# Kernel optimization log

Measured on AMD Instinct MI355X. Metric: run time of the kernel, lower is better.

Reference implementation:

```python
import jax, jax.numpy as jnp
import numpy as np

B, N, TF, DM = 16, 4096, 512, 1024

def next_fast_len(n):
    # smallest 5-smooth number >= n (matches scipy.fftpack.next_fast_len)
    while True:
        m = n
        for p in (2, 3, 5):
            while m % p == 0:
                m //= p
        if m == 1:
            return n
        n += 1

def conv1d_fft(x, weights):
    # x: (..., N, F), weights: (M,); causal exponentially-weighted correlation
    n = x.shape[-2]
    m = weights.shape[-1]
    L = next_fast_len(n + m - 1)
    f_x = jnp.fft.rfft(x, n=L, axis=-2)                 # (..., Lr, F) complex
    f_w = jnp.fft.rfft(weights, n=L, axis=-1)           # (Lr,)
    out = jnp.fft.irfft(f_x * jnp.conj(f_w)[..., None], L, axis=-2)
    out = jnp.roll(out, -1, axis=-2)
    return out[..., L - n:, :]                           # last N along seq axis

def setup_inputs() -> dict:
    key = jax.random.key(0)
    ks = jax.random.split(key, 8)
    inp = {
        "x": jax.random.normal(ks[0], (B, N, TF), dtype=jnp.float32),
        "latent_growth": jax.random.normal(ks[1], (B, N, DM), dtype=jnp.float32),
        "latent_seasonal": jax.random.normal(ks[2], (B, N, DM), dtype=jnp.float32),
        "alpha": jnp.zeros((1,), dtype=jnp.float32),  # nn.Parameter(torch.Tensor([0.0]))
        "w_growth": jax.random.normal(ks[3], (TF, DM), dtype=jnp.float32) / np.sqrt(DM),
        "b_growth": jnp.zeros((TF,), dtype=jnp.float32),
        "w_seasonal": jax.random.normal(ks[4], (TF, DM), dtype=jnp.float32) / np.sqrt(DM),
        "b_seasonal": jnp.zeros((TF,), dtype=jnp.float32),
    }
    return inp

def reference(x, latent_growth, latent_seasonal, alpha, w_growth, b_growth, w_seasonal, b_seasonal):
    n = x.shape[1]
    a = jax.nn.sigmoid(alpha)[0]
    powers = jnp.arange(n, dtype=x.dtype)[::-1]          # flipped arange
    seasonal = jnp.einsum('bnd,fd->bnf', latent_seasonal, w_seasonal) + b_seasonal
    aes_weights = a * (1.0 - a) ** powers                # alpha*(1-alpha)^k EMA kernel
    seasonal_normalized_term = conv1d_fft(x - seasonal, aes_weights)
    # NOTE: the original module computes `growth` but does not use it in the output
    growth = jnp.einsum('bnd,fd->bnf', latent_growth, w_growth) + b_growth
    growth_term = conv1d_fft(x, aes_weights)
    return seasonal_normalized_term + growth_term
```

## Files before the change

### kernel.cpp

```cpp
#include <hip/hip_runtime.h>
#include <math.h>

#define B_DIM 16
#define N_SEQ 4096
#define TF_DIM 512
#define DM_DIM 1024
#define CHUNK 128
#define NCHUNK (N_SEQ / CHUNK)
#define NKT (DM_DIM / 32)

typedef __attribute__((ext_vector_type(4))) float f32x4;
typedef __attribute__((ext_vector_type(8))) short bf16x8;
typedef unsigned short u16;
typedef unsigned int u32;

__device__ __forceinline__ u16 f2bf(float f) {
    u32 u = __builtin_bit_cast(u32, f);
    u += 0x7fffu + ((u >> 16) & 1u);
    return (u16)(u >> 16);
}

__device__ __forceinline__ void gload16(const float* g, float* l) {
    __builtin_amdgcn_global_load_lds(
        (const __attribute__((address_space(1))) void*)g,
        (__attribute__((address_space(3))) void*)l,
        16, 0, 0);
}

__device__ __forceinline__ u32 cvtpk(float lo, float hi) {
    u32 r;
    asm("v_cvt_pk_bf16_f32 %0, %1, %2" : "=v"(r) : "v"(lo), "v"(hi));
    return r;
}

__device__ __forceinline__ bf16x8 pack8(f32x4 v0, f32x4 v1) {
    union { u32 u[4]; bf16x8 v; } p;
    p.u[0] = cvtpk(v0[0], v0[1]);
    p.u[1] = cvtpk(v0[2], v0[3]);
    p.u[2] = cvtpk(v1[0], v1[1]);
    p.u[3] = cvtpk(v1[2], v1[3]);
    return p.v;
}

__global__ __launch_bounds__(256, 2)
void gemm_u_kernel(const float* __restrict__ x,
                   const float* __restrict__ ls,
                   const float* __restrict__ wmat,
                   const float* __restrict__ bias,
                   const float* __restrict__ alpha,
                   u16* __restrict__ u,
                   float* __restrict__ e)
{
    __shared__ float As[2][4096];
    __shared__ float Ws[2][4096];
    __shared__ float red[2][4][16];

    const int tid  = threadIdx.x;
    const int f0   = blockIdx.x * 128;
    const int row0 = blockIdx.y * 128;

    const int lane = tid & 63;
    const int wid  = tid >> 6;
    const int wm = wid >> 1, wn = wid & 1;
    const int l15 = lane & 15, l4 = lane >> 4;

    const int sr = wid * 32 + (lane >> 3);
    const int sc = ((lane & 7) ^ ((lane >> 3) & 7)) * 4;
    const float* aSrc = ls   + (size_t)(row0 + sr) * DM_DIM + sc;
    const float* wSrc = wmat + (size_t)(f0   + sr) * DM_DIM + sc;
    const int ldsb = wid * 1024;

#define STAGE(BUF, KT) do {                                              \
        const int _ko = (KT) * 32;                                       \
        gload16(aSrc + _ko,         &As[BUF][ldsb]);                     \
        gload16(aSrc + _ko +  8192, &As[BUF][ldsb + 256]);               \
        gload16(aSrc + _ko + 16384, &As[BUF][ldsb + 512]);               \
        gload16(aSrc + _ko + 24576, &As[BUF][ldsb + 768]);               \
        gload16(wSrc + _ko,         &Ws[BUF][ldsb]);                     \
        gload16(wSrc + _ko +  8192, &Ws[BUF][ldsb + 256]);               \
        gload16(wSrc + _ko + 16384, &Ws[BUF][ldsb + 512]);               \
        gload16(wSrc + _ko + 24576, &Ws[BUF][ldsb + 768]);               \
    } while (0)

    const int xr   = (l15 & 7) << 2;
    const int aoff = (wm * 64 + l15) * 32 + ((l4 * 8) ^ xr);
    const int woff = (wn * 64 + l15) * 32 + ((l4 * 8) ^ xr);

    f32x4 acc[4][4];
#pragma unroll
    for (int i = 0; i < 4; ++i)
#pragma unroll
        for (int j = 0; j < 4; ++j) acc[i][j] = (f32x4){0.f, 0.f, 0.f, 0.f};

#define COMPUTE(BUF) do {                                                \
        const float* _Ab = &As[BUF][0];                                  \
        const float* _Wb = &Ws[BUF][0];                                  \
        bf16x8 _af[4], _wf[4];                                           \
        _Pragma("unroll")                                                \
        for (int i = 0; i < 4; ++i) {                                    \
            f32x4 _v0 = *(const f32x4*)(_Ab + (aoff + i * 512));         \
            f32x4 _v1 = *(const f32x4*)(_Ab + ((aoff ^ 4) + i * 512));   \
            _af[i] = pack8(_v0, _v1);                                    \
        }                                                                \
        _Pragma("unroll")                                                \
        for (int i = 0; i < 4; ++i) {                                    \
            f32x4 _v0 = *(const f32x4*)(_Wb + (woff + i * 512));         \
            f32x4 _v1 = *(const f32x4*)(_Wb + ((woff ^ 4) + i * 512));   \
            _wf[i] = pack8(_v0, _v1);                                    \
        }                                                                \
        _Pragma("unroll")                                                \
        for (int mi = 0; mi < 4; ++mi)                                   \
        _Pragma("unroll")                                                \
        for (int ni = 0; ni < 4; ++ni)                                   \
            acc[mi][ni] = __builtin_amdgcn_mfma_f32_16x16x32_bf16(       \
                _af[mi], _wf[ni], acc[mi][ni], 0, 0, 0);                 \
    } while (0)

    STAGE(0, 0);
    __syncthreads();

#pragma unroll 1
    for (int kt = 0; kt < NKT; kt += 2) {
        if (kt + 1 < NKT) STAGE(1, kt + 1);
        COMPUTE(0);
        __syncthreads();
        if (kt + 2 < NKT) STAGE(0, kt + 2);
        COMPUTE(1);
        __syncthreads();
    }

    const float a = 1.0f / (1.0f + expf(-alpha[0]));
    const float c = 1.0f - a;
    const float l2c = log2f(c);

    float bia[4];
#pragma unroll
    for (int ni = 0; ni < 4; ++ni) bia[ni] = bias[f0 + wn * 64 + ni * 16 + l15];

    float epart[4] = {0.f, 0.f, 0.f, 0.f};

#pragma unroll
    for (int mi = 0; mi < 4; ++mi) {
#pragma unroll
        for (int j = 0; j < 4; ++j) {
            const int r = wm * 64 + mi * 16 + l4 * 4 + j;
            const size_t rb = (size_t)(row0 + r) * TF_DIM;
            const float wgt = (r == CHUNK - 1)
                                  ? a
                                  : a * exp2f((float)(CHUNK - 1 - r) * l2c);
#pragma unroll
            for (int ni = 0; ni < 4; ++ni) {
                const int f = f0 + wn * 64 + ni * 16 + l15;
                const float uval = 2.0f * x[rb + f] - (acc[mi][ni][j] + bia[ni]);
                u[rb + f] = f2bf(uval);
                epart[ni] = fmaf(wgt, uval, epart[ni]);
            }
        }
    }

#pragma unroll
    for (int ni = 0; ni < 4; ++ni) {
        epart[ni] += __shfl_xor(epart[ni], 16, 64);
        epart[ni] += __shfl_xor(epart[ni], 32, 64);
    }
    if (wm == 1 && l4 == 0) {
#pragma unroll
        for (int ni = 0; ni < 4; ++ni) red[wn][ni][l15] = epart[ni];
    }
    __syncthreads();
    if (wm == 0 && l4 == 0) {
#pragma unroll
        for (int ni = 0; ni < 4; ++ni) {
            const int f = f0 + wn * 64 + ni * 16 + l15;
            e[(size_t)blockIdx.y * TF_DIM + f] = epart[ni] + red[wn][ni][l15];
        }
    }
}

__global__ __launch_bounds__(256)
void ema_carry(const float* __restrict__ e, const float* __restrict__ alpha,
               float* __restrict__ carry)
{
    const int idx = blockIdx.x * 256 + threadIdx.x;
    const int f = idx & (TF_DIM - 1);
    const int b = idx >> 9;
    const float a = 1.0f / (1.0f + expf(-alpha[0]));
    const float c = 1.0f - a;
    const float cC = exp2f((float)CHUNK * log2f(c));
    const size_t base = (size_t)b * NCHUNK * TF_DIM + f;
    float Y = 0.0f;
    carry[base] = 0.0f;
    for (int ch = 1; ch < NCHUNK; ++ch) {
        Y = fmaf(cC, Y, e[base + (size_t)(ch - 1) * TF_DIM]);
        carry[base + (size_t)ch * TF_DIM] = Y;
    }
}

__global__ __launch_bounds__(256)
void ema_apply(const u16* __restrict__ u, const float* __restrict__ carry,
               const float* __restrict__ alpha, float* __restrict__ out)
{
    const int bc = blockIdx.x;
    const int tid = threadIdx.x;
    const float a = 1.0f / (1.0f + expf(-alpha[0]));
    const float c = 1.0f - a;
    float y0 = carry[(size_t)bc * TF_DIM + 2 * tid];
    float y1 = carry[(size_t)bc * TF_DIM + 2 * tid + 1];
    const u32* up = (const u32*)(u + (size_t)bc * CHUNK * TF_DIM) + tid;
    float2*    op = (float2*)(out + (size_t)bc * CHUNK * TF_DIM) + tid;
#pragma unroll 4
    for (int j = 0; j < CHUNK; ++j) {
        const u32 w = up[(size_t)j * (TF_DIM / 2)];
        const float u0 = __builtin_bit_cast(float, (w & 0xffffu) << 16);
        const float u1 = __builtin_bit_cast(float, (w >> 16) << 16);
        y0 = fmaf(c, y0, a * u0);
        y1 = fmaf(c, y1, a * u1);
        op[(size_t)j * (TF_DIM / 2)] = make_float2(y0, y1);
    }
}

extern "C" void kernel_launch(void* const* d_in, const int* in_sizes, int n_in,
                              void* d_out, int out_size, void* d_ws, size_t ws_size,
                              hipStream_t stream) {
    const float* x     = (const float*)d_in[0];
    const float* ls    = (const float*)d_in[2];
    const float* alpha = (const float*)d_in[3];
    const float* wmat  = (const float*)d_in[6];
    const float* bias  = (const float*)d_in[7];
    float* out = (float*)d_out;

    u16*   u     = (u16*)d_ws;
    float* e     = (float*)(u + (size_t)B_DIM * N_SEQ * TF_DIM);
    float* carry = e + (size_t)B_DIM * NCHUNK * TF_DIM;

    dim3 g1(TF_DIM / 128, B_DIM * N_SEQ / 128);
    gemm_u_kernel<<<g1, 256, 0, stream>>>(x, ls, wmat, bias, alpha, u, e);

    ema_carry<<<(B_DIM * TF_DIM) / 256, 256, 0, stream>>>(e, alpha, carry);
    ema_apply<<<B_DIM * NCHUNK, 256, 0, stream>>>(u, carry, alpha, out);
}
```

Baseline: 279.0 us.

## Pre-convert GEMM operands to bf16 in a separate pass and remap block order

Adds a conversion kernel that writes latent_seasonal and the seasonal weight matrix as bf16 into workspace. The GEMM then streams bf16 tiles directly into LDS with a new swizzle, dropping the per-iteration fp32-to-bf16 packing and halving LDS and global traffic inside the main loop. Blocks are linearised and remapped so groups of eight row tiles share the four feature tiles, for better L2 reuse of activation rows. Barriers become explicit vmcnt drains. The cost is an extra full pass that reads 256MB of fp32 activations and writes 128MB of bf16, which may outweigh the savings in a GEMM that is bandwidth-bound on reading those activations.

```diff
diff --git a/kernel.cpp b/kernel.cpp
--- a/kernel.cpp
+++ b/kernel.cpp
@@ -20,71 +20,93 @@
     return (u16)(u >> 16);
 }
 
-__device__ __forceinline__ void gload16(const float* g, float* l) {
-    __builtin_amdgcn_global_load_lds(
-        (const __attribute__((address_space(1))) void*)g,
-        (__attribute__((address_space(3))) void*)l,
-        16, 0, 0);
-}
-
 __device__ __forceinline__ u32 cvtpk(float lo, float hi) {
     u32 r;
     asm("v_cvt_pk_bf16_f32 %0, %1, %2" : "=v"(r) : "v"(lo), "v"(hi));
     return r;
 }
 
-__device__ __forceinline__ bf16x8 pack8(f32x4 v0, f32x4 v1) {
-    union { u32 u[4]; bf16x8 v; } p;
-    p.u[0] = cvtpk(v0[0], v0[1]);
-    p.u[1] = cvtpk(v0[2], v0[3]);
-    p.u[2] = cvtpk(v1[0], v1[1]);
-    p.u[3] = cvtpk(v1[2], v1[3]);
-    return p.v;
+__device__ __forceinline__ void gload16(const u16* g, u16* l) {
+    __builtin_amdgcn_global_load_lds(
+        (const __attribute__((address_space(1))) void*)g,
+        (__attribute__((address_space(3))) void*)l, 16, 0, 0);
+}
+
+#define SYNC_DRAIN() asm volatile("s_waitcnt vmcnt(0)\n\ts_barrier" ::: "memory")
+
+__global__ __launch_bounds__(256)
+void cvt_bf16(const float* __restrict__ ls, const float* __restrict__ wm,
+              u16* __restrict__ lsb, u16* __restrict__ wmb)
+{
+    const size_t LSG = (size_t)B_DIM * N_SEQ * DM_DIM / 4;
+    const size_t i = (size_t)blockIdx.x * 256 + threadIdx.x;
+    const float* src;
+    u16* dst;
+    if (i < LSG) { src = ls + i * 4; dst = lsb + i * 4; }
+    else         { const size_t j = i - LSG; src = wm + j * 4; dst = wmb + j * 4; }
+    const f32x4 v = *(const f32x4*)src;
+    u32* d = (u32*)dst;
+    d[0] = cvtpk(v[0], v[1]);
+    d[1] = cvtpk(v[2], v[3]);
 }
 
 __global__ __launch_bounds__(256, 2)
 void gemm_u_kernel(const float* __restrict__ x,
-                   const float* __restrict__ ls,
-                   const float* __restrict__ wmat,
+                   const u16* __restrict__ lsb,
+                   const u16* __restrict__ wmb,
                    const float* __restrict__ bias,
                    const float* __restrict__ alpha,
                    u16* __restrict__ u,
                    float* __restrict__ e)
 {
-    __shared__ float As[2][4096];
-    __shared__ float Ws[2][4096];
+    __shared__ u16 As[2][4096];
+    __shared__ u16 Ws[2][4096];
     __shared__ float red[2][4][16];
 
-    const int tid  = threadIdx.x;
-    const int f0   = blockIdx.x * 128;
-    const int row0 = blockIdx.y * 128;
+    const int tid = threadIdx.x;
+
+    const int s  = blockIdx.x;
+    const int kk = s >> 3;
+    const int fb = kk & 3;
+    const int rp = (s & 7) + ((kk >> 2) << 3);
+    const int f0   = fb * 128;
+    const int row0 = rp * 128;
 
     const int lane = tid & 63;
     const int wid  = tid >> 6;
     const int wm = wid >> 1, wn = wid & 1;
     const int l15 = lane & 15, l4 = lane >> 4;
 
-    const int sr = wid * 32 + (lane >> 3);
-    const int sc = ((lane & 7) ^ ((lane >> 3) & 7)) * 4;
-    const float* aSrc = ls   + (size_t)(row0 + sr) * DM_DIM + sc;
-    const float* wSrc = wmat + (size_t)(f0   + sr) * DM_DIM + sc;
-    const int ldsb = wid * 1024;
+    const int G0 = wid * 128 + lane;
+    const int G1 = G0 + 64;
+    int row_a, slot_a, row_b, slot_b;
+    { const int r = G0 >> 2;
+      row_a  = (r & ~1) | ((r ^ (G0 >> 4)) & 1);
+      slot_a = (G0 & 3) ^ (row_a & 3); }
+    { const int r = G1 >> 2;
+      row_b  = (r & ~1) | ((r ^ (G1 >> 4)) & 1);
+      slot_b = (G1 & 3) ^ (row_b & 3); }
+
+    const u16* aSrc0 = lsb + (size_t)(row0 + row_a) * DM_DIM + slot_a * 8;
+    const u16* aSrc1 = lsb + (size_t)(row0 + row_b) * DM_DIM + slot_b * 8;
+    const u16* wSrc0 = wmb + (size_t)(f0 + row_a) * DM_DIM + slot_a * 8;
+    const u16* wSrc1 = wmb + (size_t)(f0 + row_b) * DM_DIM + slot_b * 8;
 
 #define STAGE(BUF, KT) do {                                              \
-        const int _ko = (KT) * 32;                                       \
-        gload16(aSrc + _ko,         &As[BUF][ldsb]);                     \
-        gload16(aSrc + _ko +  8192, &As[BUF][ldsb + 256]);               \
-        gload16(aSrc + _ko + 16384, &As[BUF][ldsb + 512]);               \
-        gload16(aSrc + _ko + 24576, &As[BUF][ldsb + 768]);               \
-        gload16(wSrc + _ko,         &Ws[BUF][ldsb]);                     \
-        gload16(wSrc + _ko +  8192, &Ws[BUF][ldsb + 256]);               \
-        gload16(wSrc + _ko + 16384, &Ws[BUF][ldsb + 512]);               \
-        gload16(wSrc + _ko + 24576, &Ws[BUF][ldsb + 768]);               \
+        const int _o = (KT) * 32;                                        \
+        gload16(aSrc0 + _o, &As[BUF][wid * 1024]);                       \
+        gload16(aSrc1 + _o, &As[BUF][wid * 1024 + 512]);                 \
+        gload16(wSrc0 + _o, &Ws[BUF][wid * 1024]);                       \
+        gload16(wSrc1 + _o, &Ws[BUF][wid * 1024 + 512]);                 \
     } while (0)
 
-    const int xr   = (l15 & 7) << 2;
-    const int aoff = (wm * 64 + l15) * 32 + ((l4 * 8) ^ xr);
-    const int woff = (wn * 64 + l15) * 32 + ((l4 * 8) ^ xr);
+    int rofa[4], rofw[4];
+    const int rxor = (l15 & 7) << 3;
+#pragma unroll
+    for (int i = 0; i < 4; ++i) {
+        rofa[i] = ((wm * 64 + i * 16 + l15) * 32 + l4 * 8) ^ rxor;
+        rofw[i] = ((wn * 64 + i * 16 + l15) * 32 + l4 * 8) ^ rxor;
+    }
 
     f32x4 acc[4][4];
 #pragma unroll
@@ -93,20 +115,13 @@
         for (int j = 0; j < 4; ++j) acc[i][j] = (f32x4){0.f, 0.f, 0.f, 0.f};
 
 #define COMPUTE(BUF) do {                                                \
-        const float* _Ab = &As[BUF][0];                                  \
-        const float* _Wb = &Ws[BUF][0];                                  \
+        const u16* _Ab = As[BUF];                                        \
+        const u16* _Wb = Ws[BUF];                                        \
         bf16x8 _af[4], _wf[4];                                           \
         _Pragma("unroll")                                                \
         for (int i = 0; i < 4; ++i) {                                    \
-            f32x4 _v0 = *(const f32x4*)(_Ab + (aoff + i * 512));         \
-            f32x4 _v1 = *(const f32x4*)(_Ab + ((aoff ^ 4) + i * 512));   \
-            _af[i] = pack8(_v0, _v1);                                    \
-        }                                                                \
-        _Pragma("unroll")                                                \
-        for (int i = 0; i < 4; ++i) {                                    \
-            f32x4 _v0 = *(const f32x4*)(_Wb + (woff + i * 512));         \
-            f32x4 _v1 = *(const f32x4*)(_Wb + ((woff ^ 4) + i * 512));   \
-            _wf[i] = pack8(_v0, _v1);                                    \
+            _af[i] = *(const bf16x8*)(_Ab + rofa[i]);                    \
+            _wf[i] = *(const bf16x8*)(_Wb + rofw[i]);                    \
         }                                                                \
         _Pragma("unroll")                                                \
         for (int mi = 0; mi < 4; ++mi)                                   \
@@ -117,16 +132,17 @@
     } while (0)
 
     STAGE(0, 0);
-    __syncthreads();
+    SYNC_DRAIN();
 
 #pragma unroll 1
     for (int kt = 0; kt < NKT; kt += 2) {
         if (kt + 1 < NKT) STAGE(1, kt + 1);
         COMPUTE(0);
-        __syncthreads();
+        SYNC_DRAIN();
+
         if (kt + 2 < NKT) STAGE(0, kt + 2);
         COMPUTE(1);
-        __syncthreads();
+        SYNC_DRAIN();
     }
 
     const float a = 1.0f / (1.0f + expf(-alpha[0]));
@@ -172,7 +188,7 @@
 #pragma unroll
         for (int ni = 0; ni < 4; ++ni) {
             const int f = f0 + wn * 64 + ni * 16 + l15;
-            e[(size_t)blockIdx.y * TF_DIM + f] = epart[ni] + red[wn][ni][l15];
+            e[(size_t)rp * TF_DIM + f] = epart[ni] + red[wn][ni][l15];
         }
     }
 }
@@ -230,11 +246,15 @@
     float* out = (float*)d_out;
 
     u16*   u     = (u16*)d_ws;
-    float* e     = (float*)(u + (size_t)B_DIM * N_SEQ * TF_DIM);
+    u16*   lsb   = u + (size_t)B_DIM * N_SEQ * TF_DIM;
+    u16*   wmb   = lsb + (size_t)B_DIM * N_SEQ * DM_DIM;
+    float* e     = (float*)(wmb + (size_t)TF_DIM * DM_DIM);
     float* carry = e + (size_t)B_DIM * NCHUNK * TF_DIM;
 
-    dim3 g1(TF_DIM / 128, B_DIM * N_SEQ / 128);
-    gemm_u_kernel<<<g1, 256, 0, stream>>>(x, ls, wmat, bias, alpha, u, e);
+    const int cvt_blocks = (B_DIM * N_SEQ * DM_DIM / 4 + TF_DIM * DM_DIM / 4) / 256;
+    cvt_bf16<<<cvt_blocks, 256, 0, stream>>>(ls, wmat, lsb, wmb);
+
+    gemm_u_kernel<<<2048, 256, 0, stream>>>(x, lsb, wmb, bias, alpha, u, e);
 
     ema_carry<<<(B_DIM * TF_DIM) / 256, 256, 0, stream>>>(e, alpha, carry);
     ema_apply<<<B_DIM * NCHUNK, 256, 0, stream>>>(u, carry, alpha, out);
```

New measurement: 253.3 us. 9.2% less time.
